# Optimization experiments

Hardware: AMD Instinct MI355X
Metric: run time of the kernel (lower is better)

Reference implementation:

```python
import jax, jax.numpy as jnp
import numpy as np

INPUT_SIZE = 4096
HIDDEN_SIZE = 4096


def setup_inputs() -> dict:
    key = jax.random.key(0)
    ks = jax.random.split(key, 11)
    H, I = HIDDEN_SIZE, INPUT_SIZE
    inp = {
        "x": jax.random.normal(ks[0], (I,), dtype=jnp.float32),
        "h_prev": jax.random.normal(ks[1], (H,), dtype=jnp.float32),
        "c_prev": jax.random.normal(ks[2], (H,), dtype=jnp.float32),
        # input weights (torch init: randn)
        "W_ii": jax.random.normal(ks[3], (H, I), dtype=jnp.float32),
        "W_if": jax.random.normal(ks[4], (H, I), dtype=jnp.float32),
        "W_ig": jax.random.normal(ks[5], (H, I), dtype=jnp.float32),
        "W_io": jax.random.normal(ks[6], (H, I), dtype=jnp.float32),
        # hidden weights
        "W_hi": jax.random.normal(ks[7], (H, H), dtype=jnp.float32),
        "W_hf": jax.random.normal(ks[8], (H, H), dtype=jnp.float32),
        "W_hg": jax.random.normal(ks[9], (H, H), dtype=jnp.float32),
        "W_ho": jax.random.normal(ks[10], (H, H), dtype=jnp.float32),
        # biases (torch init: zeros)
        "b_ii": jnp.zeros((H,), jnp.float32),
        "b_if": jnp.zeros((H,), jnp.float32),
        "b_ig": jnp.zeros((H,), jnp.float32),
        "b_io": jnp.zeros((H,), jnp.float32),
        "b_hi": jnp.zeros((H,), jnp.float32),
        "b_hf": jnp.zeros((H,), jnp.float32),
        "b_hg": jnp.zeros((H,), jnp.float32),
        "b_ho": jnp.zeros((H,), jnp.float32),
    }
    return inp


def reference(x, h_prev, c_prev,
              W_ii, W_if, W_ig, W_io,
              W_hi, W_hf, W_hg, W_ho,
              b_ii, b_if, b_ig, b_io,
              b_hi, b_hf, b_hg, b_ho):
    # Fuse the 8 GEMVs into 2 GEMMs over concatenated gate weights.
    Wi = jnp.concatenate([W_ii, W_if, W_ig, W_io], axis=0)  # [4H, I]
    Wh = jnp.concatenate([W_hi, W_hf, W_hg, W_ho], axis=0)  # [4H, H]
    b = jnp.concatenate([b_ii + b_hi, b_if + b_hf, b_ig + b_hg, b_io + b_ho])
    z = Wi @ x + Wh @ h_prev + b  # [4H]
    H = h_prev.shape[0]
    i_t = jax.nn.sigmoid(z[0 * H:1 * H])
    f_t = jax.nn.sigmoid(z[1 * H:2 * H])
    g_t = jnp.tanh(z[2 * H:3 * H])
    o_t = jax.nn.sigmoid(z[3 * H:4 * H])
    c_t = f_t * c_prev + i_t * g_t
    h_t = o_t * jnp.tanh(c_t)
    return (h_t, (h_t, c_t))
```

## Files before the change

kernel.cpp:

```cpp
#include <hip/hip_runtime.h>

#define HS 4096

__global__ __launch_bounds__(256) void lstm_step(
    const float* __restrict__ x,
    const float* __restrict__ hprev,
    const float* __restrict__ cprev,
    const float* __restrict__ Wii, const float* __restrict__ Wif,
    const float* __restrict__ Wig, const float* __restrict__ Wio,
    const float* __restrict__ Whi, const float* __restrict__ Whf,
    const float* __restrict__ Whg, const float* __restrict__ Who,
    const float* __restrict__ bii, const float* __restrict__ bif_,
    const float* __restrict__ big_, const float* __restrict__ bio,
    const float* __restrict__ bhi, const float* __restrict__ bhf,
    const float* __restrict__ bhg, const float* __restrict__ bho,
    float* __restrict__ out, int mode)
{
  __shared__ float4 sx[HS / 4];
  __shared__ float4 sh[HS / 4];
  const int tid = threadIdx.x;
  const float4* gx = (const float4*)x;
  const float4* gh = (const float4*)hprev;
#pragma unroll
  for (int c = 0; c < 4; ++c) {
    sx[tid + 256 * c] = gx[tid + 256 * c];
    sh[tid + 256 * c] = gh[tid + 256 * c];
  }
  __syncthreads();

  const int wave = tid >> 6;
  const int lane = tid & 63;
  const int row = (blockIdx.x << 2) + wave;

  const float* Wx[4] = {Wii, Wif, Wig, Wio};
  const float* Wh[4] = {Whi, Whf, Whg, Who};
  float acc[4];
#pragma unroll
  for (int g = 0; g < 4; ++g) {
    float a = 0.f;
    const float4* wr = (const float4*)(Wx[g]) + (size_t)row * (HS / 4);
    const float4* hr = (const float4*)(Wh[g]) + (size_t)row * (HS / 4);
#pragma unroll
    for (int j = 0; j < 16; ++j) {
      const float4 w = wr[(j << 6) + lane];
      const float4 v = sx[(j << 6) + lane];
      a = fmaf(w.x, v.x, a);
      a = fmaf(w.y, v.y, a);
      a = fmaf(w.z, v.z, a);
      a = fmaf(w.w, v.w, a);
    }
#pragma unroll
    for (int j = 0; j < 16; ++j) {
      const float4 w = hr[(j << 6) + lane];
      const float4 v = sh[(j << 6) + lane];
      a = fmaf(w.x, v.x, a);
      a = fmaf(w.y, v.y, a);
      a = fmaf(w.z, v.z, a);
      a = fmaf(w.w, v.w, a);
    }
    acc[g] = a;
  }

#pragma unroll
  for (int g = 0; g < 4; ++g) {
#pragma unroll
    for (int off = 32; off > 0; off >>= 1)
      acc[g] += __shfl_xor(acc[g], off, 64);
  }

  if (lane == 0) {
    const float zi = acc[0] + bii[row] + bhi[row];
    const float zf = acc[1] + bif_[row] + bhf[row];
    const float zg = acc[2] + big_[row] + bhg[row];
    const float zo = acc[3] + bio[row] + bho[row];
    const float it = 1.f / (1.f + __expf(-zi));
    const float ft = 1.f / (1.f + __expf(-zf));
    const float gt = tanhf(zg);
    const float ot = 1.f / (1.f + __expf(-zo));
    const float ct = ft * cprev[row] + it * gt;
    const float ht = ot * tanhf(ct);
    out[row] = ht;
    if (mode >= 3) {
      out[HS + row] = ht;
      out[2 * HS + row] = ct;
    } else if (mode == 2) {
      out[HS + row] = ct;
    }
  }
}

extern "C" void kernel_launch(void* const* d_in, const int* in_sizes, int n_in,
                              void* d_out, int out_size, void* d_ws, size_t ws_size,
                              hipStream_t stream) {
  const float* p[19];
  for (int i = 0; i < 19; ++i) p[i] = (const float*)d_in[i];
  const int mode = out_size / HS;
  lstm_step<<<HS / 4, 256, 0, stream>>>(
      p[0], p[1], p[2],
      p[3], p[4], p[5], p[6],
      p[7], p[8], p[9], p[10],
      p[11], p[12], p[13], p[14],
      p[15], p[16], p[17], p[18],
      (float*)d_out, mode);
}
```

Baseline: 454.7 us.

## Split each row's K dimension across two waves and interleave all eight weight streams

Doubles the block to 512 threads so each row is handled by two waves, each covering half of the K dimension. Partial sums are combined through shared memory after a second barrier. The inner loop now issues loads from all eight weight matrices together, putting more memory requests in flight per wave to better saturate HBM bandwidth on this memory-bound GEMV. The cost is an extra barrier, a shared-memory reduction step, and more live registers per thread.

```diff
diff --git a/kernel.cpp b/kernel.cpp
--- a/kernel.cpp
+++ b/kernel.cpp
@@ -1,8 +1,9 @@
 #include <hip/hip_runtime.h>
 
 #define HS 4096
+#define HS4 (HS / 4)
 
-__global__ __launch_bounds__(256) void lstm_step(
+__global__ __launch_bounds__(512, 8) void lstm_step(
     const float* __restrict__ x,
     const float* __restrict__ hprev,
     const float* __restrict__ cprev,
@@ -16,75 +17,109 @@
     const float* __restrict__ bhg, const float* __restrict__ bho,
     float* __restrict__ out, int mode)
 {
-  __shared__ float4 sx[HS / 4];
-  __shared__ float4 sh[HS / 4];
+  __shared__ float4 sx[HS4];
+  __shared__ float4 sh[HS4];
+  __shared__ float part[8][8];
+
   const int tid = threadIdx.x;
-  const float4* gx = (const float4*)x;
-  const float4* gh = (const float4*)hprev;
-#pragma unroll
-  for (int c = 0; c < 4; ++c) {
-    sx[tid + 256 * c] = gx[tid + 256 * c];
-    sh[tid + 256 * c] = gh[tid + 256 * c];
+  {
+    const float4* gx = (const float4*)x;
+    const float4* gh = (const float4*)hprev;
+    sx[tid] = gx[tid];
+    sx[tid + 512] = gx[tid + 512];
+    sh[tid] = gh[tid];
+    sh[tid + 512] = gh[tid + 512];
   }
   __syncthreads();
 
-  const int wave = tid >> 6;
   const int lane = tid & 63;
-  const int row = (blockIdx.x << 2) + wave;
+  const int wid = __builtin_amdgcn_readfirstlane(tid >> 6);
+  const int rloc = wid >> 1;
+  const int khalf = wid & 1;
+  const int row = (blockIdx.x << 2) + rloc;
+  const int vbase = khalf << 9;
+  const size_t wb = (size_t)row * HS4 + vbase;
 
-  const float* Wx[4] = {Wii, Wif, Wig, Wio};
-  const float* Wh[4] = {Whi, Whf, Whg, Who};
-  float acc[4];
+  const float4* __restrict__ W0 = (const float4*)Wii + wb;
+  const float4* __restrict__ W1 = (const float4*)Wif + wb;
+  const float4* __restrict__ W2 = (const float4*)Wig + wb;
+  const float4* __restrict__ W3 = (const float4*)Wio + wb;
+  const float4* __restrict__ W4 = (const float4*)Whi + wb;
+  const float4* __restrict__ W5 = (const float4*)Whf + wb;
+  const float4* __restrict__ W6 = (const float4*)Whg + wb;
+  const float4* __restrict__ W7 = (const float4*)Who + wb;
+
+  float a0 = 0.f, a1 = 0.f, a2 = 0.f, a3 = 0.f;
+  float a4 = 0.f, a5 = 0.f, a6 = 0.f, a7 = 0.f;
+
 #pragma unroll
-  for (int g = 0; g < 4; ++g) {
-    float a = 0.f;
-    const float4* wr = (const float4*)(Wx[g]) + (size_t)row * (HS / 4);
-    const float4* hr = (const float4*)(Wh[g]) + (size_t)row * (HS / 4);
-#pragma unroll
-    for (int j = 0; j < 16; ++j) {
-      const float4 w = wr[(j << 6) + lane];
-      const float4 v = sx[(j << 6) + lane];
-      a = fmaf(w.x, v.x, a);
-      a = fmaf(w.y, v.y, a);
-      a = fmaf(w.z, v.z, a);
-      a = fmaf(w.w, v.w, a);
-    }
-#pragma unroll
-    for (int j = 0; j < 16; ++j) {
-      const float4 w = hr[(j << 6) + lane];
-      const float4 v = sh[(j << 6) + lane];
-      a = fmaf(w.x, v.x, a);
-      a = fmaf(w.y, v.y, a);
-      a = fmaf(w.z, v.z, a);
-      a = fmaf(w.w, v.w, a);
-    }
-    acc[g] = a;
+  for (int j = 0; j < 8; ++j) {
+    const int idx = (j << 6) + lane;
+    const float4 vx = sx[vbase + idx];
+    const float4 vh = sh[vbase + idx];
+    const float4 w0 = W0[idx];
+    const float4 w1 = W1[idx];
+    const float4 w2 = W2[idx];
+    const float4 w3 = W3[idx];
+    const float4 w4 = W4[idx];
+    const float4 w5 = W5[idx];
+    const float4 w6 = W6[idx];
+    const float4 w7 = W7[idx];
+    a0 = fmaf(w0.x, vx.x, a0); a0 = fmaf(w0.y, vx.y, a0);
+    a0 = fmaf(w0.z, vx.z, a0); a0 = fmaf(w0.w, vx.w, a0);
+    a1 = fmaf(w1.x, vx.x, a1); a1 = fmaf(w1.y, vx.y, a1);
+    a1 = fmaf(w1.z, vx.z, a1); a1 = fmaf(w1.w, vx.w, a1);
+    a2 = fmaf(w2.x, vx.x, a2); a2 = fmaf(w2.y, vx.y, a2);
+    a2 = fmaf(w2.z, vx.z, a2); a2 = fmaf(w2.w, vx.w, a2);
+    a3 = fmaf(w3.x, vx.x, a3); a3 = fmaf(w3.y, vx.y, a3);
+    a3 = fmaf(w3.z, vx.z, a3); a3 = fmaf(w3.w, vx.w, a3);
+    a4 = fmaf(w4.x, vh.x, a4); a4 = fmaf(w4.y, vh.y, a4);
+    a4 = fmaf(w4.z, vh.z, a4); a4 = fmaf(w4.w, vh.w, a4);
+    a5 = fmaf(w5.x, vh.x, a5); a5 = fmaf(w5.y, vh.y, a5);
+    a5 = fmaf(w5.z, vh.z, a5); a5 = fmaf(w5.w, vh.w, a5);
+    a6 = fmaf(w6.x, vh.x, a6); a6 = fmaf(w6.y, vh.y, a6);
+    a6 = fmaf(w6.z, vh.z, a6); a6 = fmaf(w6.w, vh.w, a6);
+    a7 = fmaf(w7.x, vh.x, a7); a7 = fmaf(w7.y, vh.y, a7);
+    a7 = fmaf(w7.z, vh.z, a7); a7 = fmaf(w7.w, vh.w, a7);
   }
 
+  float acc[8] = {a0, a1, a2, a3, a4, a5, a6, a7};
 #pragma unroll
-  for (int g = 0; g < 4; ++g) {
+  for (int g = 0; g < 8; ++g) {
 #pragma unroll
     for (int off = 32; off > 0; off >>= 1)
       acc[g] += __shfl_xor(acc[g], off, 64);
   }
 
   if (lane == 0) {
-    const float zi = acc[0] + bii[row] + bhi[row];
-    const float zf = acc[1] + bif_[row] + bhf[row];
-    const float zg = acc[2] + big_[row] + bhg[row];
-    const float zo = acc[3] + bio[row] + bho[row];
+#pragma unroll
+    for (int g = 0; g < 8; ++g) part[wid][g] = acc[g];
+  }
+  __syncthreads();
+
+  if (tid < 4) {
+    const int r = (blockIdx.x << 2) + tid;
+    const int w = tid << 1;
+    const float zi = part[w][0] + part[w + 1][0] + part[w][4] + part[w + 1][4]
+                     + bii[r] + bhi[r];
+    const float zf = part[w][1] + part[w + 1][1] + part[w][5] + part[w + 1][5]
+                     + bif_[r] + bhf[r];
+    const float zg = part[w][2] + part[w + 1][2] + part[w][6] + part[w + 1][6]
+                     + big_[r] + bhg[r];
+    const float zo = part[w][3] + part[w + 1][3] + part[w][7] + part[w + 1][7]
+                     + bio[r] + bho[r];
     const float it = 1.f / (1.f + __expf(-zi));
     const float ft = 1.f / (1.f + __expf(-zf));
     const float gt = tanhf(zg);
     const float ot = 1.f / (1.f + __expf(-zo));
-    const float ct = ft * cprev[row] + it * gt;
+    const float ct = ft * cprev[r] + it * gt;
     const float ht = ot * tanhf(ct);
-    out[row] = ht;
+    out[r] = ht;
     if (mode >= 3) {
-      out[HS + row] = ht;
-      out[2 * HS + row] = ct;
+      out[HS + r] = ht;
+      out[2 * HS + r] = ct;
     } else if (mode == 2) {
-      out[HS + row] = ct;
+      out[HS + r] = ct;
     }
   }
 }
@@ -95,7 +130,7 @@
   const float* p[19];
   for (int i = 0; i < 19; ++i) p[i] = (const float*)d_in[i];
   const int mode = out_size / HS;
-  lstm_step<<<HS / 4, 256, 0, stream>>>(
+  lstm_step<<<HS / 4, 512, 0, stream>>>(
       p[0], p[1], p[2],
       p[3], p[4], p[5], p[6],
       p[7], p[8], p[9], p[10],
```

Result: slower. 468.3 us (+3.0%).

## Interleave eight gate weight streams with register double-buffered prefetch

Applied to the files above, without the earlier changes.

Restructures the per-row GEMV loop so all eight gate weight rows are walked together, with the next float4 of each row and of the shared input vectors loaded into registers while the current one is multiplied. Each gate now has two partial accumulators (input and hidden) that are summed before the wave reduction. A launch-bounds occupancy hint is added. The aim is more outstanding memory loads per wave to better saturate HBM, at the cost of higher register pressure.

```diff
diff --git a/kernel.cpp b/kernel.cpp
--- a/kernel.cpp
+++ b/kernel.cpp
@@ -1,8 +1,9 @@
 #include <hip/hip_runtime.h>
 
 #define HS 4096
+#define HS4 (HS / 4)
 
-__global__ __launch_bounds__(256) void lstm_step(
+__global__ __launch_bounds__(256, 4) void lstm_step(
     const float* __restrict__ x,
     const float* __restrict__ hprev,
     const float* __restrict__ cprev,
@@ -16,51 +17,81 @@
     const float* __restrict__ bhg, const float* __restrict__ bho,
     float* __restrict__ out, int mode)
 {
-  __shared__ float4 sx[HS / 4];
-  __shared__ float4 sh[HS / 4];
+  __shared__ float4 sx[HS4];
+  __shared__ float4 sh[HS4];
   const int tid = threadIdx.x;
-  const float4* gx = (const float4*)x;
-  const float4* gh = (const float4*)hprev;
+  {
+    const float4* gx = (const float4*)x;
+    const float4* gh = (const float4*)hprev;
 #pragma unroll
-  for (int c = 0; c < 4; ++c) {
-    sx[tid + 256 * c] = gx[tid + 256 * c];
-    sh[tid + 256 * c] = gh[tid + 256 * c];
+    for (int c = 0; c < 4; ++c) {
+      sx[tid + 256 * c] = gx[tid + 256 * c];
+      sh[tid + 256 * c] = gh[tid + 256 * c];
+    }
   }
   __syncthreads();
 
-  const int wave = tid >> 6;
   const int lane = tid & 63;
-  const int row = (blockIdx.x << 2) + wave;
+  const int wid = __builtin_amdgcn_readfirstlane(tid >> 6);
+  const int row = (blockIdx.x << 2) + wid;
+  const size_t wb = (size_t)row * HS4;
 
-  const float* Wx[4] = {Wii, Wif, Wig, Wio};
-  const float* Wh[4] = {Whi, Whf, Whg, Who};
-  float acc[4];
+  const float4* __restrict__ W0 = (const float4*)Wii + wb;
+  const float4* __restrict__ W1 = (const float4*)Wif + wb;
+  const float4* __restrict__ W2 = (const float4*)Wig + wb;
+  const float4* __restrict__ W3 = (const float4*)Wio + wb;
+  const float4* __restrict__ W4 = (const float4*)Whi + wb;
+  const float4* __restrict__ W5 = (const float4*)Whf + wb;
+  const float4* __restrict__ W6 = (const float4*)Whg + wb;
+  const float4* __restrict__ W7 = (const float4*)Who + wb;
+
+  float a0 = 0.f, a1 = 0.f, a2 = 0.f, a3 = 0.f;
+  float a4 = 0.f, a5 = 0.f, a6 = 0.f, a7 = 0.f;
+
+  float4 cw0 = W0[lane], cw1 = W1[lane], cw2 = W2[lane], cw3 = W3[lane];
+  float4 cw4 = W4[lane], cw5 = W5[lane], cw6 = W6[lane], cw7 = W7[lane];
+  float4 cvx = sx[lane], cvh = sh[lane];
+
 #pragma unroll
-  for (int g = 0; g < 4; ++g) {
-    float a = 0.f;
-    const float4* wr = (const float4*)(Wx[g]) + (size_t)row * (HS / 4);
-    const float4* hr = (const float4*)(Wh[g]) + (size_t)row * (HS / 4);
-#pragma unroll
-    for (int j = 0; j < 16; ++j) {
-      const float4 w = wr[(j << 6) + lane];
-      const float4 v = sx[(j << 6) + lane];
-      a = fmaf(w.x, v.x, a);
-      a = fmaf(w.y, v.y, a);
-      a = fmaf(w.z, v.z, a);
-      a = fmaf(w.w, v.w, a);
+  for (int j = 0; j < 16; ++j) {
+    const int nidx = ((j + 1) << 6) + lane;
+    float4 nw0, nw1, nw2, nw3, nw4, nw5, nw6, nw7, nvx, nvh;
+    if (j < 15) {
+      nvx = sx[nidx];
+      nvh = sh[nidx];
+      nw0 = W0[nidx];
+      nw1 = W1[nidx];
+      nw2 = W2[nidx];
+      nw3 = W3[nidx];
+      nw4 = W4[nidx];
+      nw5 = W5[nidx];
+      nw6 = W6[nidx];
+      nw7 = W7[nidx];
     }
-#pragma unroll
-    for (int j = 0; j < 16; ++j) {
-      const float4 w = hr[(j << 6) + lane];
-      const float4 v = sh[(j << 6) + lane];
-      a = fmaf(w.x, v.x, a);
-      a = fmaf(w.y, v.y, a);
-      a = fmaf(w.z, v.z, a);
-      a = fmaf(w.w, v.w, a);
+    a0 = fmaf(cw0.x, cvx.x, a0); a0 = fmaf(cw0.y, cvx.y, a0);
+    a0 = fmaf(cw0.z, cvx.z, a0); a0 = fmaf(cw0.w, cvx.w, a0);
+    a1 = fmaf(cw1.x, cvx.x, a1); a1 = fmaf(cw1.y, cvx.y, a1);
+    a1 = fmaf(cw1.z, cvx.z, a1); a1 = fmaf(cw1.w, cvx.w, a1);
+    a2 = fmaf(cw2.x, cvx.x, a2); a2 = fmaf(cw2.y, cvx.y, a2);
+    a2 = fmaf(cw2.z, cvx.z, a2); a2 = fmaf(cw2.w, cvx.w, a2);
+    a3 = fmaf(cw3.x, cvx.x, a3); a3 = fmaf(cw3.y, cvx.y, a3);
+    a3 = fmaf(cw3.z, cvx.z, a3); a3 = fmaf(cw3.w, cvx.w, a3);
+    a4 = fmaf(cw4.x, cvh.x, a4); a4 = fmaf(cw4.y, cvh.y, a4);
+    a4 = fmaf(cw4.z, cvh.z, a4); a4 = fmaf(cw4.w, cvh.w, a4);
+    a5 = fmaf(cw5.x, cvh.x, a5); a5 = fmaf(cw5.y, cvh.y, a5);
+    a5 = fmaf(cw5.z, cvh.z, a5); a5 = fmaf(cw5.w, cvh.w, a5);
+    a6 = fmaf(cw6.x, cvh.x, a6); a6 = fmaf(cw6.y, cvh.y, a6);
+    a6 = fmaf(cw6.z, cvh.z, a6); a6 = fmaf(cw6.w, cvh.w, a6);
+    a7 = fmaf(cw7.x, cvh.x, a7); a7 = fmaf(cw7.y, cvh.y, a7);
+    a7 = fmaf(cw7.z, cvh.z, a7); a7 = fmaf(cw7.w, cvh.w, a7);
+    if (j < 15) {
+      cw0 = nw0; cw1 = nw1; cw2 = nw2; cw3 = nw3;
+      cw4 = nw4; cw5 = nw5; cw6 = nw6; cw7 = nw7;
+      cvx = nvx; cvh = nvh;
     }
-    acc[g] = a;
   }
 
+  float acc[4] = {a0 + a4, a1 + a5, a2 + a6, a3 + a7};
 #pragma unroll
   for (int g = 0; g < 4; ++g) {
 #pragma unroll
```

New measurement: 454.1 us. No clear change (-0.1%).
